# Performance work log

Measured on AMD Instinct MI355X. Metric: run time of the kernel, lower is better.

The kernel has to match this reference:

```python
import jax, jax.numpy as jnp
import numpy as np
from jax.scipy.linalg import cho_solve

# Nearly-constant-velocity model constants (4-dim state: [x, y, vx, vy])
NCV_Q = np.array([[1/3, 0.0, 1/2, 0.0],
                  [0.0, 1/3, 0.0, 1/2],
                  [1/2, 0.0, 1.0, 0.0],
                  [0.0, 1/2, 0.0, 1.0]], dtype=np.float32)
NCV_F = np.array([[1.0, 0.0, 0.0, 0.0],
                  [0.0, 1.0, 0.0, 0.0],
                  [1.0, 0.0, 1.0, 0.0],
                  [0.0, 1.0, 0.0, 1.0]], dtype=np.float32)

NUM_SENSORS = 64
T = 2000


def setup_inputs() -> dict:
    key = jax.random.key(0)
    observations = jax.random.normal(key, (T, 2 * NUM_SENSORS), dtype=jnp.float32)
    return {
        "observations": observations,
        "log_bias_scale": jnp.zeros((), jnp.float32),
        "log_obs_noise": jnp.zeros((), jnp.float32),
        "log_trans_noise": jnp.zeros((), jnp.float32),
    }


def reference(observations, log_bias_scale, log_obs_noise, log_trans_noise):
    """Exact Gaussian belief propagation of the funsor model, expressed as an
    augmented-state Kalman filter. Latent = [state(4), bias(obs_dim)] where bias
    is constant over time. Returns (log evidence, posterior mean and cov of the
    final 4-dim state with bias marginalized out) == (logp.data, posterior)."""
    obs_dim = observations.shape[-1]
    ns = obs_dim // 2
    d = 4 + obs_dim  # augmented latent dim

    # scale_tril = s * M  =>  covariance = s^2 * M @ M.T
    bias_var = jnp.exp(2.0 * log_bias_scale)
    obs_var = jnp.exp(2.0 * log_obs_noise)
    trans_var = jnp.exp(2.0 * log_trans_noise)

    # Transition: curr_mean = prev @ F  <=>  mean = F.T @ prev ; bias is constant.
    A = jnp.zeros((d, d), jnp.float32).at[:4, :4].set(NCV_F.T).at[4:, 4:].set(jnp.eye(obs_dim, dtype=jnp.float32))
    Q = jnp.zeros((d, d), jnp.float32).at[:4, :4].set(trans_var * NCV_Q)

    # observation_matrix = eye(4,2).unsqueeze(-1).expand(-1,-1,ns).reshape(4,-1)
    OM = jnp.reshape(jnp.broadcast_to(jnp.eye(4, 2, dtype=jnp.float32)[:, :, None], (4, 2, ns)), (4, obs_dim))
    # obs_loc = state @ OM + bias  =>  H_aug = [OM.T | I]
    H = jnp.concatenate([OM.T, jnp.eye(obs_dim, dtype=jnp.float32)], axis=1)  # (obs_dim, d)
    R = obs_var * jnp.eye(obs_dim, dtype=jnp.float32)

    # Priors: state ~ N(0, (100 I)(100 I)^T = 1e4 I); bias ~ N(0, bias_scale^2 I)
    m0 = jnp.zeros((d,), jnp.float32)
    P0 = jnp.diag(jnp.concatenate([jnp.full((4,), 1e4, jnp.float32),
                                   bias_var * jnp.ones((obs_dim,), jnp.float32)]))

    log2pi = jnp.log(jnp.asarray(2.0 * np.pi, jnp.float32))

    def step(carry, y):
        m, P = carry
        # predict
        m = A @ m
        P = A @ P @ A.T + Q
        # innovation
        HP = H @ P                      # (obs_dim, d)
        S = HP @ H.T + R                # (obs_dim, obs_dim)
        L = jnp.linalg.cholesky(S)
        r = y - H @ m
        alpha = cho_solve((L, True), r)
        ll = -0.5 * (r @ alpha) - jnp.sum(jnp.log(jnp.diag(L))) - 0.5 * obs_dim * log2pi
        # update: K = P H^T S^{-1} = (S^{-1} H P)^T
        K = cho_solve((L, True), HP).T  # (d, obs_dim)
        m = m + K @ r
        P = P - K @ HP
        P = 0.5 * (P + P.T)
        return (m, P), ll

    (m, P), lls = jax.lax.scan(step, (m0, P0), observations)
    logp = jnp.sum(lls)
    post_mean = m[:4]
    post_cov = P[:4, :4]
    return logp, post_mean, post_cov
```

## Files before the change

### kernel.cpp

```cpp
#include <hip/hip_runtime.h>
#include <math.h>

#define TT 2000
#define T0 16
#define NREM (TT - T0)
#define CH 31
#define NTAIL 32
#define NPART 33
#define WS_PART 4096
#define PART_STRIDE 132
#define WS_TOKS 8452
#define WS_TOKC 8484
#define WS_FLOATS 8544
#define MAGIC32 0x5E11F00Du

#if defined(__has_builtin)
#if __has_builtin(__builtin_amdgcn_rcpf)
#define FRCP(x) __builtin_amdgcn_rcpf(x)
#endif
#endif
#ifndef FRCP
#define FRCP(x) (1.0f / (x))
#endif

#define LOG2PI_F 1.8378770664093453f

#define AST(p, v) __hip_atomic_store((p), (v), __ATOMIC_RELAXED, __HIP_MEMORY_SCOPE_AGENT)
#define ALD(p)    __hip_atomic_load((p), __ATOMIC_RELAXED, __HIP_MEMORY_SCOPE_AGENT)
#define WAITVM()  asm volatile("s_waitcnt vmcnt(0)" ::: "memory")

__device__ __forceinline__ void mmul3(const float* __restrict__ a,
                                      const float* __restrict__ b,
                                      float* __restrict__ c) {
#pragma unroll
    for (int r = 0; r < 3; ++r)
#pragma unroll
        for (int cc = 0; cc < 3; ++cc)
            c[3*r+cc] = a[3*r+0]*b[0+cc] + a[3*r+1]*b[3+cc] + a[3*r+2]*b[6+cc];
}

__global__ __launch_bounds__(256) void kf_one(const float* __restrict__ obs,
                                              float* __restrict__ ws,
                                              const float* __restrict__ p_lbs,
                                              const float* __restrict__ p_lon,
                                              const float* __restrict__ p_ltn,
                                              float* __restrict__ out) {
    __shared__ float s_lds[2][2048];
    __shared__ float colpart[128];
    __shared__ float sh_sq[2];
    __shared__ float sh_heads[2];
    __shared__ float sh_tailzz[2];
    __shared__ float sh_csum[2];
    __shared__ float sh_s2c[2];
    __shared__ float frz[14];
    __shared__ float mst[2][3];
    __shared__ float Wm[6][9];
    __shared__ float wred[2];
    __shared__ float vfin[2][3];
    __shared__ float sh_hll[4];

    const int tid  = threadIdx.x;
    const int lane = tid & 63;
    const int wave = tid >> 6;
    const float4* obs4 = reinterpret_cast<const float4*>(obs);
    unsigned int* tok_s = reinterpret_cast<unsigned int*>(ws + WS_TOKS);
    unsigned int* tok_c = reinterpret_cast<unsigned int*>(ws + WS_TOKC);

    if (blockIdx.x != 0) {
        const int q = tid & 31, rho = tid >> 5, g = q >> 4;
        if (tid < 128) colpart[tid] = 0.0f;
        if (tid < 2)   sh_sq[tid]   = 0.0f;

        if (blockIdx.x <= NTAIL) {
            const int jp = blockIdx.x - 1;
            const int row0 = T0 + jp*62;
            float4 v[8];
            bool act[8];
#pragma unroll
            for (int i = 0; i < 8; ++i) {
                const int rr = i*8 + rho;
                act[i] = (rr < 62);
                v[i] = act[i] ? obs4[(row0 + rr)*32 + q]
                              : make_float4(0.f, 0.f, 0.f, 0.f);
            }
            float c0=0.f, c1=0.f, c2=0.f, c3=0.f, sq=0.f;
#pragma unroll
            for (int i = 0; i < 8; ++i) {
                if (!act[i]) continue;
                c0 += v[i].x; c1 += v[i].y; c2 += v[i].z; c3 += v[i].w;
                sq += v[i].x*v[i].x + v[i].y*v[i].y + v[i].z*v[i].z + v[i].w*v[i].w;
                float s = (v[i].x + v[i].y) + (v[i].z + v[i].w);
                s += __shfl_xor(s, 1);
                s += __shfl_xor(s, 2);
                s += __shfl_xor(s, 4);
                s += __shfl_xor(s, 8);
                if ((q & 15) == 0) AST(&ws[g*2048 + row0 + i*8 + rho], s);
            }
            WAITVM();
            __syncthreads();
            if (tid == 0) AST(&tok_s[jp], MAGIC32);

            atomicAdd(&colpart[4*q+0], c0);
            atomicAdd(&colpart[4*q+1], c1);
            atomicAdd(&colpart[4*q+2], c2);
            atomicAdd(&colpart[4*q+3], c3);
            atomicAdd(&sh_sq[g], sq);
            __syncthreads();
            if (wave == 0) {
                float* part = ws + WS_PART + jp*PART_STRIDE;
                AST(&part[lane], colpart[lane]);
                AST(&part[64 + lane], colpart[64 + lane]);
                if (lane < 2) AST(&part[128 + lane], sh_sq[lane]);
                WAITVM();
                if (lane == 0) AST(&tok_c[jp], MAGIC32);
            }
        } else {
            float4 v[2];
#pragma unroll
            for (int i = 0; i < T0/8; ++i) v[i] = obs4[(i*8 + rho)*32 + q];
            float c0=0.f, c1=0.f, c2=0.f, c3=0.f, sq=0.f;
#pragma unroll
            for (int i = 0; i < T0/8; ++i) {
                c0 += v[i].x; c1 += v[i].y; c2 += v[i].z; c3 += v[i].w;
                sq += v[i].x*v[i].x + v[i].y*v[i].y + v[i].z*v[i].z + v[i].w*v[i].w;
            }
            __syncthreads();
            atomicAdd(&colpart[4*q+0], c0);
            atomicAdd(&colpart[4*q+1], c1);
            atomicAdd(&colpart[4*q+2], c2);
            atomicAdd(&colpart[4*q+3], c3);
            atomicAdd(&sh_sq[g], sq);
            __syncthreads();
            if (wave == 0) {
                float* part = ws + WS_PART + 32*PART_STRIDE;
                AST(&part[lane], colpart[lane]);
                AST(&part[64 + lane], colpart[64 + lane]);
                if (lane < 2) AST(&part[128 + lane], sh_sq[lane]);
                WAITVM();
                if (lane == 0) AST(&tok_c[32], MAGIC32);
            }
        }
        return;
    }

    {
        const int q = tid & 31, rho = tid >> 5, g = q >> 4;
        float4 v[2];
#pragma unroll
        for (int i = 0; i < T0/8; ++i) v[i] = obs4[(i*8 + rho)*32 + q];
#pragma unroll
        for (int i = 0; i < T0/8; ++i) {
            float s = (v[i].x + v[i].y) + (v[i].z + v[i].w);
            s += __shfl_xor(s, 1);
            s += __shfl_xor(s, 2);
            s += __shfl_xor(s, 4);
            s += __shfl_xor(s, 8);
            if ((q & 15) == 0) s_lds[g][i*8 + rho] = s;
        }
    }
    __syncthreads();

    const float sb2 = expf(2.0f * p_lbs[0]);
    const float so2 = expf(2.0f * p_lon[0]);
    const float tv  = expf(2.0f * p_ltn[0]);

    float Ppp = 10000.f, Ppv = 0.f, PpB = 0.f, Pvv = 10000.f, PvB = 0.f, PBB = sb2;

    if (wave == 0) {
        if (tid < 2) {
            const float tv3  = tv * (1.0f/3.0f);
            const float tv2h = tv * 0.5f;
            float p = 0.f, vvel = 0.f, B = 0.f;
            float acc_r2 = 0.f, acc_lS = 0.f;
            const float4* zr4 = reinterpret_cast<const float4*>(&s_lds[tid][0]);
            float4 zc = zr4[0];
            for (int bk = 0; bk < T0/4; ++bk) {
                const float4 zn = (bk < T0/4 - 1) ? zr4[bk+1] : zc;
#pragma unroll
                for (int u = 0; u < 4; ++u) {
                    const float zraw = (u==0) ? zc.x : (u==1) ? zc.y : (u==2) ? zc.z : zc.w;
                    p += vvel;
                    Ppp += 2.0f*Ppv + Pvv + tv3;
                    Ppv += Pvv + tv2h;
                    PpB += PvB;
                    Pvv += tv;
                    const float z   = zraw * 0.125f;
                    const float Php = 8.0f*Ppp + PpB;
                    const float Phv = 8.0f*Ppv + PvB;
                    const float PhB = 8.0f*PpB + PBB;
                    const float S   = 8.0f*Php + PhB + so2;
                    const float r   = z - (8.0f*p + B);
                    const float inv = FRCP(S);
                    acc_r2 += r*r*inv;
                    acc_lS += __logf(S);
                    const float kp = Php*inv, kv = Phv*inv, kB_ = PhB*inv;
                    p    += kp*r; vvel += kv*r; B += kB_*r;
                    Ppp -= kp*Php; Ppv -= kp*Phv; PpB -= kp*PhB;
                    Pvv -= kv*Phv; PvB -= kv*PhB; PBB -= kB_*PhB;
                }
                zc = zn;
            }
            mst[tid][0] = p; mst[tid][1] = vvel; mst[tid][2] = B;
            sh_hll[tid]     = acc_r2;
            sh_hll[2 + tid] = acc_lS;
        }
    } else if (wave == 2) {
        if (lane == 0) {
            float P2p = 10000.f, P2v = 0.f, P2B = 0.f, V2 = 10000.f, VB2 = 0.f, BB2 = sb2;
            const float tv3  = tv * (1.0f/3.0f);
            const float tv2h = tv * 0.5f;
            for (int t = 0; t < T0; ++t) {
                P2p += 2.0f*P2v + V2 + tv3;
                P2v += V2 + tv2h;
                P2B += VB2;
                V2  += tv;
                const float Php = 8.0f*P2p + P2B;
                const float Phv = 8.0f*P2v + VB2;
                const float PhB = 8.0f*P2B + BB2;
                const float S   = 8.0f*Php + PhB + so2;
                const float inv = FRCP(S);
                const float kp = Php*inv, kv = Phv*inv, kB_ = PhB*inv;
                P2p -= kp*Php; P2v -= kp*Phv; P2B -= kp*PhB;
                V2  -= kv*Phv; VB2 -= kv*PhB; BB2 -= kB_*PhB;
            }
            const float Ap  = P2p + 2.0f*P2v + V2 + tv*(1.0f/3.0f);
            const float Apv = P2v + V2 + tv*0.5f;
            const float ApB = P2B + VB2;
            const float AvB = VB2;
            const float AB  = BB2;
            const float Php = 8.0f*Ap  + ApB;
            const float Phv = 8.0f*Apv + AvB;
            const float PhB = 8.0f*ApB + AB;
            const float S   = 8.0f*Php + PhB + so2;
            const float inv = FRCP(S);
            const float K0 = Php*inv, K1 = Phv*inv, K2 = PhB*inv;
            frz[0] = 1.0f - 8.0f*K0; frz[1] = 1.0f - 8.0f*K0; frz[2] = -K0;
            frz[3] =      - 8.0f*K1; frz[4] = 1.0f - 8.0f*K1; frz[5] = -K1;
            frz[6] =      - 8.0f*K2; frz[7] =      - 8.0f*K2; frz[8] = 1.0f - K2;
            frz[9] = K0; frz[10] = K1; frz[11] = K2; frz[12] = S;
            float A1[9];
#pragma unroll
            for (int k = 0; k < 9; ++k) A1[k] = frz[k];
            float A2[9], A4[9], A8[9], A16[9], A24[9], A28[9], A30[9], W[9], Wn[9];
            mmul3(A1, A1, A2);
            mmul3(A2, A2, A4);
            mmul3(A4, A4, A8);
            mmul3(A8, A8, A16);
            mmul3(A16, A8, A24);
            mmul3(A24, A4, A28);
            mmul3(A28, A2, A30);
            mmul3(A30, A1, W);
#pragma unroll
            for (int k = 0; k < 9; ++k) Wm[0][k] = W[k];
            for (int st = 1; st < 6; ++st) {
                mmul3(W, W, Wn);
#pragma unroll
                for (int k = 0; k < 9; ++k) { Wm[st][k] = Wn[k]; W[k] = Wn[k]; }
            }
        }
    } else {
        bool ready = false;
        do {
            unsigned int v = (lane < NTAIL) ? ALD(&tok_s[lane]) : MAGIC32;
            ready = (bool)__all(v == MAGIC32);
        } while (!ready);
        const unsigned long long* wsu = reinterpret_cast<const unsigned long long*>(ws);
        unsigned long long* su = reinterpret_cast<unsigned long long*>(&s_lds[0][0]);
        const int base = (wave == 1) ? lane : (64 + lane);
#pragma unroll
        for (int i = 0; i < 16; ++i) {
            const int j = base + 128*i;
            if (j < 1984) {
                const int g = (j >= 992) ? 1 : 0;
                const int m = j - g*992;
                const int idx = g*1024 + T0/2 + m;
                su[idx] = ALD(&wsu[idx]);
            }
        }
    }
    __syncthreads();

    const float a00 = frz[0], a01 = frz[1], a02 = frz[2];
    const float a10 = frz[3], a11 = frz[4], a12 = frz[5];
    const float a20 = frz[6], a21 = frz[7], a22 = frz[8];
    const float k0r = frz[9], k1r = frz[10], k2r = frz[11];
    const float Sfz = frz[12];
    const int g2 = wave;
    const int tbase = T0 + lane*CH;

    if (tid < 128) {
        float cx = 0.f, cy = 0.f, cz = 0.f;
        float gx = 8.f, gy = 8.f, gz = 1.f;
        float qa = 0.f, qb0 = 0.f, qb1 = 0.f, qb2 = 0.f;
        float qc00 = 0.f, qc01 = 0.f, qc02 = 0.f, qc11 = 0.f, qc12 = 0.f, qc22 = 0.f;
        float tzz = 0.f;
        for (int k = 0; k < CH; ++k) {
            const float z = s_lds[g2][tbase + k] * 0.125f;
            tzz += z*z;
            const float e = z - (8.0f*(cx + cy) + cz);
            qa  += e*e;
            qb0 += e*gx; qb1 += e*gy; qb2 += e*gz;
            qc00 += gx*gx; qc01 += gx*gy; qc02 += gx*gz;
            qc11 += gy*gy; qc12 += gy*gz; qc22 += gz*gz;
            const float nx = a00*cx + a01*cy + a02*cz + k0r*z;
            const float ny = a10*cx + a11*cy + a12*cz + k1r*z;
            const float nz = a20*cx + a21*cy + a22*cz + k2r*z;
            const float ngx = gx*a00 + gy*a10 + gz*a20;
            const float ngy = gx*a01 + gy*a11 + gz*a21;
            const float ngz = gx*a02 + gy*a12 + gz*a22;
            cx = nx; cy = ny; cz = nz;
            gx = ngx; gy = ngy; gz = ngz;
        }
        if (lane == 0) {
            const float mx0 = mst[g2][0], my0 = mst[g2][1], mz0 = mst[g2][2];
            cx += Wm[0][0]*mx0 + Wm[0][1]*my0 + Wm[0][2]*mz0;
            cy += Wm[0][3]*mx0 + Wm[0][4]*my0 + Wm[0][5]*mz0;
            cz += Wm[0][6]*mx0 + Wm[0][7]*my0 + Wm[0][8]*mz0;
        }
#pragma unroll
        for (int st = 0; st < 6; ++st) {
            const int s = 1 << st;
            float px = __shfl_up(cx, s);
            float py = __shfl_up(cy, s);
            float pz = __shfl_up(cz, s);
            if (lane < s) { px = 0.f; py = 0.f; pz = 0.f; }
            cx += Wm[st][0]*px + Wm[st][1]*py + Wm[st][2]*pz;
            cy += Wm[st][3]*px + Wm[st][4]*py + Wm[st][5]*pz;
            cz += Wm[st][6]*px + Wm[st][7]*py + Wm[st][8]*pz;
        }
        if (lane == 63) { vfin[g2][0] = cx; vfin[g2][1] = cy; vfin[g2][2] = cz; }
        float mx = __shfl_up(cx, 1);
        float my = __shfl_up(cy, 1);
        float mz = __shfl_up(cz, 1);
        if (lane == 0) { mx = mst[g2][0]; my = mst[g2][1]; mz = mst[g2][2]; }
        float rs = qa
                 - 2.0f*(qb0*mx + qb1*my + qb2*mz)
                 + (qc00*mx*mx + qc11*my*my + qc22*mz*mz
                    + 2.0f*(qc01*mx*my + qc02*mx*mz + qc12*my*mz));
#pragma unroll
        for (int m = 1; m < 64; m <<= 1) {
            rs  += __shfl_xor(rs, m);
            tzz += __shfl_xor(tzz, m);
        }
        if (lane == 0) { wred[g2] = rs; sh_tailzz[g2] = tzz; }
    } else if (wave == 2) {
        bool ready = false;
        do {
            unsigned int v = (lane < NPART) ? ALD(&tok_c[lane]) : MAGIC32;
            ready = (bool)__all(v == MAGIC32);
        } while (!ready);
        const int c4 = lane & 31;
        const int par = lane >> 5;
        const unsigned long long* pu =
            reinterpret_cast<const unsigned long long*>(ws + WS_PART);
        float t0 = 0.f, t1 = 0.f, t2 = 0.f, t3 = 0.f;
        for (int b = par; b < NPART; b += 2) {
            const unsigned long long lo = ALD(&pu[b*66 + 2*c4]);
            const unsigned long long hi = ALD(&pu[b*66 + 2*c4 + 1]);
            t0 += __uint_as_float((unsigned int)lo);
            t1 += __uint_as_float((unsigned int)(lo >> 32));
            t2 += __uint_as_float((unsigned int)hi);
            t3 += __uint_as_float((unsigned int)(hi >> 32));
        }
        t0 += __shfl_xor(t0, 32);
        t1 += __shfl_xor(t1, 32);
        t2 += __shfl_xor(t2, 32);
        t3 += __shfl_xor(t3, 32);
        float csum = (t0 + t1) + (t2 + t3);
        float s2   = t0*t0 + t1*t1 + t2*t2 + t3*t3;
#pragma unroll
        for (int m = 1; m < 16; m <<= 1) {
            csum += __shfl_xor(csum, m);
            s2   += __shfl_xor(s2, m);
        }
        if (lane == 0)  { sh_csum[0] = csum; sh_s2c[0] = s2; }
        if (lane == 16) { sh_csum[1] = csum; sh_s2c[1] = s2; }
    } else {
        float hq0 = 0.f, hq1 = 0.f;
        if (lane < T0) {
            const float a = s_lds[0][lane], b = s_lds[1][lane];
            hq0 = a*a; hq1 = b*b;
        }
#pragma unroll
        for (int m = 1; m < 64; m <<= 1) {
            hq0 += __shfl_xor(hq0, m);
            hq1 += __shfl_xor(hq1, m);
        }
        if (lane == 0) { sh_heads[0] = hq0; sh_heads[1] = hq1; }
        bool ready = false;
        do {
            unsigned int v = (lane < NPART) ? ALD(&tok_c[lane]) : MAGIC32;
            ready = (bool)__all(v == MAGIC32);
        } while (!ready);
        float q0 = 0.f, q1 = 0.f;
        if (lane < NPART) {
            q0 = ALD(&ws[WS_PART + lane*PART_STRIDE + 128]);
            q1 = ALD(&ws[WS_PART + lane*PART_STRIDE + 129]);
        }
#pragma unroll
        for (int m = 1; m < 64; m <<= 1) {
            q0 += __shfl_xor(q0, m);
            q1 += __shfl_xor(q1, m);
        }
        if (lane == 0) { sh_sq[0] = q0; sh_sq[1] = q1; }
    }
    __syncthreads();

    if (tid == 0) {
        const double Sd = (double)Sfz;
        const double rsum = (double)wred[0] + (double)wred[1];
        const double LOG2PI = 1.8378770664093453;
        const double llrem = -0.5*rsum/Sd
                             - (double)NREM*((double)__logf(Sfz) + LOG2PI);
        const double llseq = -0.5*((double)(sh_hll[0] + sh_hll[1])
                                 + (double)(sh_hll[2] + sh_hll[3]))
                             - (double)T0*LOG2PI;

        const double ssq0 = (double)sh_heads[0] + 64.0*(double)sh_tailzz[0];
        const double ssq1 = (double)sh_heads[1] + 64.0*(double)sh_tailzz[1];
        const double Q0 = (double)sh_sq[0] - ssq0*(1.0/64.0);
        const double Q1 = (double)sh_sq[1] - ssq1*(1.0/64.0);
        const double R0 = (double)sh_s2c[0]
                        - (double)sh_csum[0]*(double)sh_csum[0]*(1.0/64.0);
        const double R1 = (double)sh_s2c[1]
                        - (double)sh_csum[1]*(double)sh_csum[1]*(1.0/64.0);
        const double Td = (double)TT;
        const double denom = (double)so2 + Td*(double)sb2;
        double ll_static = -0.5*(Q0 + Q1 - (double)sb2*(R0 + R1)/denom)/(double)so2;
        ll_static += -63.0*((Td - 1.0)*(double)__logf(so2) + (double)__logf((float)denom));
        ll_static += -63.0*Td*LOG2PI;

        out[0] = (float)(llseq + llrem + ll_static);
        out[1] = vfin[0][0]; out[2] = vfin[1][0];
        out[3] = vfin[0][1]; out[4] = vfin[1][1];
        float C[16];
#pragma unroll
        for (int i = 0; i < 16; ++i) C[i] = 0.0f;
        C[0]  = Ppp; C[2]  = Ppv; C[8]  = Ppv; C[10] = Pvv;
        C[5]  = Ppp; C[7]  = Ppv; C[13] = Ppv; C[15] = Pvv;
#pragma unroll
        for (int i = 0; i < 16; ++i) out[5+i] = C[i];
    }
}

__global__ __launch_bounds__(256) void kf_fused(
    const float* __restrict__ obs,
    const float* __restrict__ p_lbs,
    const float* __restrict__ p_lon,
    const float* __restrict__ p_ltn,
    float* __restrict__ out) {
    __shared__ float s_lds[2][2048];
    __shared__ float Ycols[128];
    __shared__ float sh_sq[2];
    __shared__ float sh_ssq[2];
    __shared__ float sh_stats[2][2];
    const int tid = threadIdx.x;
    if (tid < 128) Ycols[tid] = 0.0f;
    if (tid < 2) { sh_sq[tid] = 0.0f; sh_ssq[tid] = 0.0f; }
    __syncthreads();
    const int q = tid & 31, rho = tid >> 5, g = q >> 4;
    float c0=0.f, c1=0.f, c2=0.f, c3=0.f, sq=0.f, ssq_acc=0.f;
    const float4* obs4 = reinterpret_cast<const float4*>(obs);
    for (int i = 0; i < TT/8; ++i) {
        const int row = i*8 + rho;
        const float4 v = obs4[row*32 + q];
        c0 += v.x; c1 += v.y; c2 += v.z; c3 += v.w;
        sq += v.x*v.x + v.y*v.y + v.z*v.z + v.w*v.w;
        float s = (v.x + v.y) + (v.z + v.w);
        s += __shfl_xor(s, 1); s += __shfl_xor(s, 2);
        s += __shfl_xor(s, 4); s += __shfl_xor(s, 8);
        if ((q & 15) == 0) { s_lds[g][row] = s; ssq_acc += s*s; }
    }
    atomicAdd(&sh_sq[g], sq);
    if ((q & 15) == 0) atomicAdd(&sh_ssq[g], ssq_acc);
    atomicAdd(&Ycols[4*q+0], c0); atomicAdd(&Ycols[4*q+1], c1);
    atomicAdd(&Ycols[4*q+2], c2); atomicAdd(&Ycols[4*q+3], c3);
    __syncthreads();
    if (tid < 128) {
        const int w = tid >> 6, lane = tid & 63;
        const float y = Ycols[w*64 + lane];
        float su = y, s2 = y*y;
#pragma unroll
        for (int m = 1; m < 64; m <<= 1) { su += __shfl_xor(su, m); s2 += __shfl_xor(s2, m); }
        if (lane == 0) { sh_stats[w][0] = su; sh_stats[w][1] = s2; }
    }
    __syncthreads();
    if (tid >= 64) return;
    const float sb2 = expf(2.0f * p_lbs[0]);
    const float so2 = expf(2.0f * p_lon[0]);
    const float tv  = expf(2.0f * p_ltn[0]);
    float p = 0.f, vv = 0.f, B = 0.f;
    float Ppp = 10000.f, Ppv = 0.f, PpB = 0.f, Pvv = 10000.f, PvB = 0.f, PBB = sb2;
    double ll = 0.0;
    if (tid < 2) {
        const float tv3 = tv*(1.0f/3.0f), tv2h = tv*0.5f;
        const float* zrow = s_lds[tid];
        for (int t = 0; t < TT; ++t) {
            p += vv;
            Ppp += 2.0f*Ppv + Pvv + tv3; Ppv += Pvv + tv2h; PpB += PvB; Pvv += tv;
            const float z = zrow[t]*0.125f;
            const float Php = 8.0f*Ppp + PpB, Phv = 8.0f*Ppv + PvB, PhB = 8.0f*PpB + PBB;
            const float S = 8.0f*Php + PhB + so2;
            const float r = z - (8.0f*p + B);
            const float inv = 1.0f/S;
            ll -= 0.5 * (double)(r*r*inv + __logf(S) + LOG2PI_F);
            const float kp = Php*inv, kv = Phv*inv, kB = PhB*inv;
            p += kp*r; vv += kv*r; B += kB*r;
            Ppp -= kp*Php; Ppv -= kp*Phv; PpB -= kp*PhB;
            Pvv -= kv*Phv; PvB -= kv*PhB; PBB -= kB*PhB;
        }
    }
    const float p1 = __shfl(p, 1), v1 = __shfl(vv, 1);
    const float Ppp1 = __shfl(Ppp, 1), Ppv1 = __shfl(Ppv, 1), Pvv1 = __shfl(Pvv, 1);
    const double ll1 = __shfl(ll, 1);
    if (tid == 0) {
        const float Q0 = sh_sq[0] - sh_ssq[0]*(1.0f/64.0f);
        const float Q1 = sh_sq[1] - sh_ssq[1]*(1.0f/64.0f);
        const float R0 = sh_stats[0][1] - sh_stats[0][0]*sh_stats[0][0]*(1.0f/64.0f);
        const float R1 = sh_stats[1][1] - sh_stats[1][0]*sh_stats[1][0]*(1.0f/64.0f);
        const double DLOG2PI = 1.8378770664093453;
        const double Td = (double)TT;
        const double denom = (double)so2 + Td*(double)sb2;
        double ll_static = -0.5*((double)Q0 + (double)Q1
                                 - (double)sb2*((double)R0 + (double)R1)/denom)/(double)so2;
        ll_static += -0.5*126.0*((Td - 1.0)*log((double)so2) + log(denom));
        ll_static += -0.5*126.0*Td*DLOG2PI;
        out[0] = (float)(ll + ll1 + ll_static);
        out[1] = p; out[2] = p1; out[3] = vv; out[4] = v1;
        float C[16];
#pragma unroll
        for (int i = 0; i < 16; ++i) C[i] = 0.0f;
        C[0] = Ppp; C[2] = Ppv; C[8] = Ppv; C[10] = Pvv;
        C[5] = Ppp1; C[7] = Ppv1; C[13] = Ppv1; C[15] = Pvv1;
#pragma unroll
        for (int i = 0; i < 16; ++i) out[5+i] = C[i];
    }
}

extern "C" void kernel_launch(void* const* d_in, const int* in_sizes, int n_in,
                              void* d_out, int out_size, void* d_ws, size_t ws_size,
                              hipStream_t stream) {
    const float* obs = (const float*)d_in[0];
    const float* lbs = (const float*)d_in[1];
    const float* lon = (const float*)d_in[2];
    const float* ltn = (const float*)d_in[3];
    float* out = (float*)d_out;
    if (ws_size >= WS_FLOATS * sizeof(float)) {
        float* ws = (float*)d_ws;
        hipLaunchKernelGGL(kf_one, dim3(NTAIL + 2), dim3(256), 0, stream,
                           obs, ws, lbs, lon, ltn, out);
    } else {
        hipLaunchKernelGGL(kf_fused, dim3(1), dim3(256), 0, stream,
                           obs, lbs, lon, ltn, out);
    }
}
```

Baseline: 17.05 us.

## Restructure block-0 schedule: per-wave register loads, redundant frozen-gain compute, fewer barriers

In the coordinating block, the 16-step head filter and its sum of squares move to wave 3, with the head observations staged in a small LDS buffer. That removes the initial block-wide barrier. Waves 0/1 now read their tail chunk from the workspace straight into registers instead of copying it through a large LDS array. Each of those waves also recomputes the frozen Riccati gain itself rather than waiting on wave 2 through a barrier. The aim is to shorten the serial critical path and drop the big LDS footprint, at the cost of duplicated scalar Riccati work and higher register pressure.

```diff
diff --git a/kernel.cpp b/kernel.cpp
--- a/kernel.cpp
+++ b/kernel.cpp
@@ -39,13 +39,49 @@
             c[3*r+cc] = a[3*r+0]*b[0+cc] + a[3*r+1]*b[3+cc] + a[3*r+2]*b[6+cc];
 }
 
+__device__ __forceinline__ void ric_frozen(float sb2, float so2, float tv,
+                                           float* __restrict__ fz) {
+    float P2p = 10000.f, P2v = 0.f, P2B = 0.f, V2 = 10000.f, VB2 = 0.f, BB2 = sb2;
+    const float tv3  = tv * (1.0f/3.0f);
+    const float tv2h = tv * 0.5f;
+    for (int t = 0; t < T0; ++t) {
+        P2p += 2.0f*P2v + V2 + tv3;
+        P2v += V2 + tv2h;
+        P2B += VB2;
+        V2  += tv;
+        const float Php = 8.0f*P2p + P2B;
+        const float Phv = 8.0f*P2v + VB2;
+        const float PhB = 8.0f*P2B + BB2;
+        const float S   = 8.0f*Php + PhB + so2;
+        const float inv = FRCP(S);
+        const float kp = Php*inv, kv = Phv*inv, kB_ = PhB*inv;
+        P2p -= kp*Php; P2v -= kp*Phv; P2B -= kp*PhB;
+        V2  -= kv*Phv; VB2 -= kv*PhB; BB2 -= kB_*PhB;
+    }
+    const float Ap  = P2p + 2.0f*P2v + V2 + tv*(1.0f/3.0f);
+    const float Apv = P2v + V2 + tv*0.5f;
+    const float ApB = P2B + VB2;
+    const float AvB = VB2;
+    const float AB  = BB2;
+    const float Php = 8.0f*Ap  + ApB;
+    const float Phv = 8.0f*Apv + AvB;
+    const float PhB = 8.0f*ApB + AB;
+    const float S   = 8.0f*Php + PhB + so2;
+    const float inv = FRCP(S);
+    const float K0 = Php*inv, K1 = Phv*inv, K2 = PhB*inv;
+    fz[0] = 1.0f - 8.0f*K0; fz[1] = 1.0f - 8.0f*K0; fz[2] = -K0;
+    fz[3] =      - 8.0f*K1; fz[4] = 1.0f - 8.0f*K1; fz[5] = -K1;
+    fz[6] =      - 8.0f*K2; fz[7] =      - 8.0f*K2; fz[8] = 1.0f - K2;
+    fz[9] = K0; fz[10] = K1; fz[11] = K2; fz[12] = S;
+}
+
 __global__ __launch_bounds__(256) void kf_one(const float* __restrict__ obs,
                                               float* __restrict__ ws,
                                               const float* __restrict__ p_lbs,
                                               const float* __restrict__ p_lon,
                                               const float* __restrict__ p_ltn,
                                               float* __restrict__ out) {
-    __shared__ float s_lds[2][2048];
+    __shared__ float s_head[2][16];
     __shared__ float colpart[128];
     __shared__ float sh_sq[2];
     __shared__ float sh_heads[2];
@@ -54,6 +90,7 @@
     __shared__ float sh_s2c[2];
     __shared__ float frz[14];
     __shared__ float mst[2][3];
+    __shared__ float sh_P[3];
     __shared__ float Wm[6][9];
     __shared__ float wred[2];
     __shared__ float vfin[2][3];
@@ -143,104 +180,92 @@
         return;
     }
 
-    {
-        const int q = tid & 31, rho = tid >> 5, g = q >> 4;
-        float4 v[2];
-#pragma unroll
-        for (int i = 0; i < T0/8; ++i) v[i] = obs4[(i*8 + rho)*32 + q];
-#pragma unroll
-        for (int i = 0; i < T0/8; ++i) {
+    const float sb2 = expf(2.0f * p_lbs[0]);
+    const float so2 = expf(2.0f * p_lon[0]);
+    const float tv  = expf(2.0f * p_ltn[0]);
+
+    float cx = 0.f, cy = 0.f, cz = 0.f;
+    float qa = 0.f, qb0 = 0.f, qb1 = 0.f, qb2 = 0.f;
+    float qc00 = 0.f, qc01 = 0.f, qc02 = 0.f, qc11 = 0.f, qc12 = 0.f, qc22 = 0.f;
+    float tzz = 0.f;
+    const int g2 = wave;
+
+    if (wave == 3) {
+        const int q3 = lane & 31, rho3 = lane >> 5, g3 = q3 >> 4;
+        float4 v[8];
+#pragma unroll
+        for (int i = 0; i < 8; ++i) v[i] = obs4[(2*i + rho3)*32 + q3];
+#pragma unroll
+        for (int i = 0; i < 8; ++i) {
             float s = (v[i].x + v[i].y) + (v[i].z + v[i].w);
             s += __shfl_xor(s, 1);
             s += __shfl_xor(s, 2);
             s += __shfl_xor(s, 4);
             s += __shfl_xor(s, 8);
-            if ((q & 15) == 0) s_lds[g][i*8 + rho] = s;
-        }
-    }
-    __syncthreads();
-
-    const float sb2 = expf(2.0f * p_lbs[0]);
-    const float so2 = expf(2.0f * p_lon[0]);
-    const float tv  = expf(2.0f * p_ltn[0]);
-
-    float Ppp = 10000.f, Ppv = 0.f, PpB = 0.f, Pvv = 10000.f, PvB = 0.f, PBB = sb2;
-
-    if (wave == 0) {
-        if (tid < 2) {
+            if ((q3 & 15) == 0) s_head[g3][2*i + rho3] = s;
+        }
+        asm volatile("s_waitcnt lgkmcnt(0)" ::: "memory");
+
+        if (lane < 2) {
             const float tv3  = tv * (1.0f/3.0f);
             const float tv2h = tv * 0.5f;
             float p = 0.f, vvel = 0.f, B = 0.f;
+            float Ppp = 10000.f, Ppv = 0.f, PpB = 0.f,
+                  Pvv = 10000.f, PvB = 0.f, PBB = sb2;
             float acc_r2 = 0.f, acc_lS = 0.f;
-            const float4* zr4 = reinterpret_cast<const float4*>(&s_lds[tid][0]);
-            float4 zc = zr4[0];
-            for (int bk = 0; bk < T0/4; ++bk) {
-                const float4 zn = (bk < T0/4 - 1) ? zr4[bk+1] : zc;
-#pragma unroll
-                for (int u = 0; u < 4; ++u) {
-                    const float zraw = (u==0) ? zc.x : (u==1) ? zc.y : (u==2) ? zc.z : zc.w;
-                    p += vvel;
-                    Ppp += 2.0f*Ppv + Pvv + tv3;
-                    Ppv += Pvv + tv2h;
-                    PpB += PvB;
-                    Pvv += tv;
-                    const float z   = zraw * 0.125f;
-                    const float Php = 8.0f*Ppp + PpB;
-                    const float Phv = 8.0f*Ppv + PvB;
-                    const float PhB = 8.0f*PpB + PBB;
-                    const float S   = 8.0f*Php + PhB + so2;
-                    const float r   = z - (8.0f*p + B);
-                    const float inv = FRCP(S);
-                    acc_r2 += r*r*inv;
-                    acc_lS += __logf(S);
-                    const float kp = Php*inv, kv = Phv*inv, kB_ = PhB*inv;
-                    p    += kp*r; vvel += kv*r; B += kB_*r;
-                    Ppp -= kp*Php; Ppv -= kp*Phv; PpB -= kp*PhB;
-                    Pvv -= kv*Phv; PvB -= kv*PhB; PBB -= kB_*PhB;
-                }
-                zc = zn;
-            }
-            mst[tid][0] = p; mst[tid][1] = vvel; mst[tid][2] = B;
-            sh_hll[tid]     = acc_r2;
-            sh_hll[2 + tid] = acc_lS;
-        }
+            const float4* zr4 = reinterpret_cast<const float4*>(&s_head[lane][0]);
+            float4 zb[4];
+#pragma unroll
+            for (int i = 0; i < 4; ++i) zb[i] = zr4[i];
+#pragma unroll
+            for (int t = 0; t < T0; ++t) {
+                const float4 zq = zb[t >> 2];
+                const int u = t & 3;
+                const float zraw = (u==0) ? zq.x : (u==1) ? zq.y : (u==2) ? zq.z : zq.w;
+                p += vvel;
+                Ppp += 2.0f*Ppv + Pvv + tv3;
+                Ppv += Pvv + tv2h;
+                PpB += PvB;
+                Pvv += tv;
+                const float z   = zraw * 0.125f;
+                const float Php = 8.0f*Ppp + PpB;
+                const float Phv = 8.0f*Ppv + PvB;
+                const float PhB = 8.0f*PpB + PBB;
+                const float S   = 8.0f*Php + PhB + so2;
+                const float r   = z - (8.0f*p + B);
+                const float inv = FRCP(S);
+                acc_r2 += r*r*inv;
+                acc_lS += __logf(S);
+                const float kp = Php*inv, kv = Phv*inv, kB_ = PhB*inv;
+                p    += kp*r; vvel += kv*r; B += kB_*r;
+                Ppp -= kp*Php; Ppv -= kp*Phv; PpB -= kp*PhB;
+                Pvv -= kv*Phv; PvB -= kv*PhB; PBB -= kB_*PhB;
+            }
+            mst[lane][0] = p; mst[lane][1] = vvel; mst[lane][2] = B;
+            sh_hll[lane]     = acc_r2;
+            sh_hll[2 + lane] = acc_lS;
+            if (lane == 0) { sh_P[0] = Ppp; sh_P[1] = Ppv; sh_P[2] = Pvv; }
+        }
+        float hq0 = 0.f, hq1 = 0.f;
+        if (lane < T0) {
+            const float a = s_head[0][lane], b = s_head[1][lane];
+            hq0 = a*a; hq1 = b*b;
+        }
+#pragma unroll
+        for (int m = 1; m < 64; m <<= 1) {
+            hq0 += __shfl_xor(hq0, m);
+            hq1 += __shfl_xor(hq1, m);
+        }
+        if (lane == 0) { sh_heads[0] = hq0; sh_heads[1] = hq1; }
     } else if (wave == 2) {
         if (lane == 0) {
-            float P2p = 10000.f, P2v = 0.f, P2B = 0.f, V2 = 10000.f, VB2 = 0.f, BB2 = sb2;
-            const float tv3  = tv * (1.0f/3.0f);
-            const float tv2h = tv * 0.5f;
-            for (int t = 0; t < T0; ++t) {
-                P2p += 2.0f*P2v + V2 + tv3;
-                P2v += V2 + tv2h;
-                P2B += VB2;
-                V2  += tv;
-                const float Php = 8.0f*P2p + P2B;
-                const float Phv = 8.0f*P2v + VB2;
-                const float PhB = 8.0f*P2B + BB2;
-                const float S   = 8.0f*Php + PhB + so2;
-                const float inv = FRCP(S);
-                const float kp = Php*inv, kv = Phv*inv, kB_ = PhB*inv;
-                P2p -= kp*Php; P2v -= kp*Phv; P2B -= kp*PhB;
-                V2  -= kv*Phv; VB2 -= kv*PhB; BB2 -= kB_*PhB;
-            }
-            const float Ap  = P2p + 2.0f*P2v + V2 + tv*(1.0f/3.0f);
-            const float Apv = P2v + V2 + tv*0.5f;
-            const float ApB = P2B + VB2;
-            const float AvB = VB2;
-            const float AB  = BB2;
-            const float Php = 8.0f*Ap  + ApB;
-            const float Phv = 8.0f*Apv + AvB;
-            const float PhB = 8.0f*ApB + AB;
-            const float S   = 8.0f*Php + PhB + so2;
-            const float inv = FRCP(S);
-            const float K0 = Php*inv, K1 = Phv*inv, K2 = PhB*inv;
-            frz[0] = 1.0f - 8.0f*K0; frz[1] = 1.0f - 8.0f*K0; frz[2] = -K0;
-            frz[3] =      - 8.0f*K1; frz[4] = 1.0f - 8.0f*K1; frz[5] = -K1;
-            frz[6] =      - 8.0f*K2; frz[7] =      - 8.0f*K2; frz[8] = 1.0f - K2;
-            frz[9] = K0; frz[10] = K1; frz[11] = K2; frz[12] = S;
+            float fz[14];
+            ric_frozen(sb2, so2, tv, fz);
+#pragma unroll
+            for (int k = 0; k < 13; ++k) frz[k] = fz[k];
             float A1[9];
 #pragma unroll
-            for (int k = 0; k < 9; ++k) A1[k] = frz[k];
+            for (int k = 0; k < 9; ++k) A1[k] = fz[k];
             float A2[9], A4[9], A8[9], A16[9], A24[9], A28[9], A30[9], W[9], Wn[9];
             mmul3(A1, A1, A2);
             mmul3(A2, A2, A4);
@@ -264,38 +289,24 @@
             unsigned int v = (lane < NTAIL) ? ALD(&tok_s[lane]) : MAGIC32;
             ready = (bool)__all(v == MAGIC32);
         } while (!ready);
-        const unsigned long long* wsu = reinterpret_cast<const unsigned long long*>(ws);
-        unsigned long long* su = reinterpret_cast<unsigned long long*>(&s_lds[0][0]);
-        const int base = (wave == 1) ? lane : (64 + lane);
-#pragma unroll
-        for (int i = 0; i < 16; ++i) {
-            const int j = base + 128*i;
-            if (j < 1984) {
-                const int g = (j >= 992) ? 1 : 0;
-                const int m = j - g*992;
-                const int idx = g*1024 + T0/2 + m;
-                su[idx] = ALD(&wsu[idx]);
-            }
-        }
-    }
-    __syncthreads();
-
-    const float a00 = frz[0], a01 = frz[1], a02 = frz[2];
-    const float a10 = frz[3], a11 = frz[4], a12 = frz[5];
-    const float a20 = frz[6], a21 = frz[7], a22 = frz[8];
-    const float k0r = frz[9], k1r = frz[10], k2r = frz[11];
-    const float Sfz = frz[12];
-    const int g2 = wave;
-    const int tbase = T0 + lane*CH;
-
-    if (tid < 128) {
-        float cx = 0.f, cy = 0.f, cz = 0.f;
+
+        float sreg[CH];
+        {
+            const float* src = ws + g2*2048 + T0 + CH*lane;
+#pragma unroll
+            for (int k = 0; k < CH; ++k) sreg[k] = ALD(&src[k]);
+        }
+        float fz[14];
+        ric_frozen(sb2, so2, tv, fz);
+        const float a00 = fz[0], a01 = fz[1], a02 = fz[2];
+        const float a10 = fz[3], a11 = fz[4], a12 = fz[5];
+        const float a20 = fz[6], a21 = fz[7], a22 = fz[8];
+        const float k0r = fz[9], k1r = fz[10], k2r = fz[11];
+
         float gx = 8.f, gy = 8.f, gz = 1.f;
-        float qa = 0.f, qb0 = 0.f, qb1 = 0.f, qb2 = 0.f;
-        float qc00 = 0.f, qc01 = 0.f, qc02 = 0.f, qc11 = 0.f, qc12 = 0.f, qc22 = 0.f;
-        float tzz = 0.f;
+#pragma unroll
         for (int k = 0; k < CH; ++k) {
-            const float z = s_lds[g2][tbase + k] * 0.125f;
+            const float z = sreg[k] * 0.125f;
             tzz += z*z;
             const float e = z - (8.0f*(cx + cy) + cz);
             qa  += e*e;
@@ -311,6 +322,10 @@
             cx = nx; cy = ny; cz = nz;
             gx = ngx; gy = ngy; gz = ngz;
         }
+    }
+    __syncthreads();
+
+    if (tid < 128) {
         if (lane == 0) {
             const float mx0 = mst[g2][0], my0 = mst[g2][1], mz0 = mst[g2][2];
             cx += Wm[0][0]*mx0 + Wm[0][1]*my0 + Wm[0][2]*mz0;
@@ -376,17 +391,6 @@
         if (lane == 0)  { sh_csum[0] = csum; sh_s2c[0] = s2; }
         if (lane == 16) { sh_csum[1] = csum; sh_s2c[1] = s2; }
     } else {
-        float hq0 = 0.f, hq1 = 0.f;
-        if (lane < T0) {
-            const float a = s_lds[0][lane], b = s_lds[1][lane];
-            hq0 = a*a; hq1 = b*b;
-        }
-#pragma unroll
-        for (int m = 1; m < 64; m <<= 1) {
-            hq0 += __shfl_xor(hq0, m);
-            hq1 += __shfl_xor(hq1, m);
-        }
-        if (lane == 0) { sh_heads[0] = hq0; sh_heads[1] = hq1; }
         bool ready = false;
         do {
             unsigned int v = (lane < NPART) ? ALD(&tok_c[lane]) : MAGIC32;
@@ -407,6 +411,7 @@
     __syncthreads();
 
     if (tid == 0) {
+        const float Sfz = frz[12];
         const double Sd = (double)Sfz;
         const double rsum = (double)wred[0] + (double)wred[1];
         const double LOG2PI = 1.8378770664093453;
@@ -436,8 +441,8 @@
         float C[16];
 #pragma unroll
         for (int i = 0; i < 16; ++i) C[i] = 0.0f;
-        C[0]  = Ppp; C[2]  = Ppv; C[8]  = Ppv; C[10] = Pvv;
-        C[5]  = Ppp; C[7]  = Ppv; C[13] = Ppv; C[15] = Pvv;
+        C[0]  = sh_P[0]; C[2]  = sh_P[1]; C[8]  = sh_P[1]; C[10] = sh_P[2];
+        C[5]  = sh_P[0]; C[7]  = sh_P[1]; C[13] = sh_P[1]; C[15] = sh_P[2];
 #pragma unroll
         for (int i = 0; i < 16; ++i) out[5+i] = C[i];
     }
```

Result: slower. 18.62 us (+9.2%).
